# Performance work log

Measured on AMD Instinct MI355X. Metric: run time of the kernel, lower is better.

Reference implementation:

```python
import jax, jax.numpy as jnp
import numpy as np

D_MODEL = 1024
NUM_HEADS = 16
HEAD_WIDTH = 64
SEQ_LEN = 2048
BATCH = 2
NEG_INF = -1e9


def alibi_slopes(num_heads):
    # 2**(-i * 8/num_heads) for i = 1..num_heads, shape [H, 1, 1]
    step = 8.0 / num_heads
    i = jnp.arange(1, num_heads + 1, dtype=jnp.float32)
    return (2.0 ** (-i * step))[:, None, None]


def relative_positions(t_q, t_v):
    # matrix[i, j] = j - i, shape [t_q, t_v]
    return (jnp.arange(t_v)[None, :] - jnp.arange(t_q)[:, None]).astype(jnp.float32)


def setup_inputs() -> dict:
    key = jax.random.key(0)
    ks = jax.random.split(key, 6)
    queries = jax.random.normal(ks[0], (BATCH, SEQ_LEN, D_MODEL), dtype=jnp.float32)
    keys = jax.random.normal(ks[1], (BATCH, SEQ_LEN, D_MODEL), dtype=jnp.float32)
    values = jax.random.normal(ks[2], (BATCH, SEQ_LEN, D_MODEL), dtype=jnp.float32)
    # causal additive mask, broadcastable [1, 1, S, S]
    causal = jnp.where(
        jnp.arange(SEQ_LEN)[None, :] > jnp.arange(SEQ_LEN)[:, None], NEG_INF, 0.0
    ).astype(jnp.float32)[None, None]
    scale = 1.0 / np.sqrt(D_MODEL)
    Wq = jax.random.normal(ks[3], (D_MODEL, D_MODEL), dtype=jnp.float32) * scale
    Wk = jax.random.normal(ks[4], (D_MODEL, D_MODEL), dtype=jnp.float32) * scale
    Wv = jax.random.normal(ks[5], (D_MODEL, D_MODEL), dtype=jnp.float32) * scale
    return {"queries": queries, "keys": keys, "values": values, "mask": causal,
            "Wq": Wq, "Wk": Wk, "Wv": Wv}


def reference(queries, keys, values, mask, Wq, Wk, Wv):
    N, t_q, d = queries.shape
    _, t_v, _ = keys.shape
    H, hw = NUM_HEADS, HEAD_WIDTH

    def split_heads(x, t):
        # [N, t, d] -> [N, H, t, hw]  (nn.Linear: x @ W.T)
        return x.reshape(N, t, H, hw).transpose(0, 2, 1, 3)

    q = split_heads(queries @ Wq.T, t_q)
    k = split_heads(keys @ Wk.T, t_v)
    v = split_heads(values @ Wv.T, t_v)

    att = jnp.einsum("bhqd,bhkd->bhqk", q, k) / np.sqrt(hw)
    # ALiBi bias: slope_h * (j - i), broadcast over batch
    att = att + (alibi_slopes(H) * relative_positions(t_q, t_v))[None]
    att = att + mask[:, :, :t_q, :t_v]
    att = jax.nn.softmax(att, axis=-1)
    res = jnp.einsum("bhqk,bhkd->bhqd", att, v)  # [N, H, t_q, hw]
    return res.transpose(0, 2, 1, 3).reshape(N, t_v, d)
```

## Files before the change

### kernel.cpp

```cpp
#include <hip/hip_runtime.h>
#include <hip/hip_bf16.h>

#define BATCH 2
#define HEADS 16
#define SEQ 2048
#define HW 64
#define DMODEL 1024

typedef unsigned short u16;
typedef __attribute__((ext_vector_type(8))) short short8;
typedef __attribute__((ext_vector_type(4))) float floatx4;

typedef __attribute__((address_space(3))) void* lds_t;
typedef const __attribute__((address_space(1))) void* gbl_t;

__device__ __forceinline__ u16 f2bf(float f) {
    union { float f; unsigned int u; } v; v.f = f;
    unsigned int r = v.u + 0x7fffu + ((v.u >> 16) & 1u);
    return (u16)(r >> 16);
}

__device__ __forceinline__ unsigned int pk2bf(float a, float b) {
    union { __hip_bfloat162 h; unsigned int u; } c;
    c.h = __float22bfloat162_rn(make_float2(a, b));
    return c.u;
}

__global__ __launch_bounds__(256) void proj_kernel(
    const float* __restrict__ Xk, const float* __restrict__ Xv,
    const float* __restrict__ Wk, const float* __restrict__ Wv,
    u16* __restrict__ Ok, u16* __restrict__ Ov)
{
    const float* X; const float* W;
    if (blockIdx.z == 0) { X = Xk; W = Wk; }
    else                 { X = Xv; W = Wv; }

    __shared__ u16 As[128][72];
    __shared__ u16 Bs[128][72];

    const int tid = threadIdx.x;
    const int lane = tid & 63, wave = tid >> 6;
    const int quad = lane >> 4, l15 = lane & 15;
    const int wm = (wave >> 1) << 6, wn = (wave & 1) << 6;
    const int tm = blockIdx.y, tn = blockIdx.x;

    const int sr = tid >> 4;
    const int sc = (tid & 15) << 2;
    const float* Xp = X + (size_t)(tm * 128 + sr) * DMODEL + sc;
    const float* Wp = W + (size_t)(tn * 128 + sr) * DMODEL + sc;

    float4 ra[8], rb[8];
#define PLOAD(K0) \
    for (int i = 0; i < 8; i++) { \
        ra[i] = *reinterpret_cast<const float4*>(Xp + (size_t)16 * i * DMODEL + (K0)); \
        rb[i] = *reinterpret_cast<const float4*>(Wp + (size_t)16 * i * DMODEL + (K0)); \
    }

    floatx4 acc[4][4];
    for (int i = 0; i < 4; i++) for (int j = 0; j < 4; j++) acc[i][j] = (floatx4)0.0f;

    PLOAD(0);
    for (int k0 = 0; k0 < DMODEL; k0 += 64) {
        for (int i = 0; i < 8; i++) {
            uint2 pa; pa.x = pk2bf(ra[i].x, ra[i].y); pa.y = pk2bf(ra[i].z, ra[i].w);
            *reinterpret_cast<uint2*>(&As[sr + 16 * i][sc]) = pa;
            uint2 pb; pb.x = pk2bf(rb[i].x, rb[i].y); pb.y = pk2bf(rb[i].z, rb[i].w);
            *reinterpret_cast<uint2*>(&Bs[sr + 16 * i][sc]) = pb;
        }
        __syncthreads();
        if (k0 + 64 < DMODEL) { PLOAD(k0 + 64); }
        for (int kc = 0; kc < 2; kc++) {
            short8 af[4], bf[4];
            for (int i = 0; i < 4; i++)
                af[i] = *reinterpret_cast<const short8*>(&As[wm + i * 16 + l15][kc * 32 + quad * 8]);
            for (int j = 0; j < 4; j++)
                bf[j] = *reinterpret_cast<const short8*>(&Bs[wn + j * 16 + l15][kc * 32 + quad * 8]);
            for (int i = 0; i < 4; i++)
                for (int j = 0; j < 4; j++)
                    acc[i][j] = __builtin_amdgcn_mfma_f32_16x16x32_bf16(af[i], bf[j], acc[i][j], 0, 0, 0);
        }
        __syncthreads();
    }
#undef PLOAD

    if (blockIdx.z == 0) {
        for (int i = 0; i < 4; i++) for (int j = 0; j < 4; j++) {
            int n = (tn << 7) + wn + (j << 4) + l15;
            int h = n >> 6, d = n & 63;
            for (int r = 0; r < 4; r++) {
                int m = (tm << 7) + wm + (i << 4) + (quad << 2) + r;
                int b = m >> 11, s = m & 2047;
                int pc = (((d >> 3) ^ (s & 7)) << 3) | (d & 7);
                Ok[(size_t)((((b << 4) + h) << 11) + s) * 64 + pc] = f2bf(acc[i][j][r]);
            }
        }
    } else {
        for (int i = 0; i < 4; i++) for (int j = 0; j < 4; j++) {
            int n = (tn << 7) + wn + (j << 4) + l15;
            int h = n >> 6, d = n & 63;
            int m = (tm << 7) + wm + (i << 4) + (quad << 2);
            int b = m >> 11, s0 = m & 2047;
            int ps = (s0 & ~63) | (((((s0 >> 3) & 7) ^ (d & 7)) << 3)) | (s0 & 7);
            uint2 pk;
            pk.x = pk2bf(acc[i][j][0], acc[i][j][1]);
            pk.y = pk2bf(acc[i][j][2], acc[i][j][3]);
            *reinterpret_cast<uint2*>(Ov + ((size_t)(((b << 4) + h) << 6) + d) * SEQ + ps) = pk;
        }
    }
}

__global__ __launch_bounds__(256) void attn_kernel(
    const float* __restrict__ Xq, const float* __restrict__ Wq,
    const u16* __restrict__ K, const u16* __restrict__ VtG,
    float* __restrict__ out)
{
    __shared__ u16 smem[16896];
    u16* Pst = smem + 12288;

    const int tid = threadIdx.x;
    const int lane = tid & 63, wave = tid >> 6;
    const int quad = lane >> 4, l15 = lane & 15;

    const int bid = blockIdx.x;
    const int qt = 31 - (bid >> 5);
    const int bh = bid & 31;
    const int b = bh >> 4, h = bh & 15;
    const float slope = exp2f(-0.5f * (float)(h + 1));
    const int q0 = qt << 6;

    const u16* Kh  = K   + (size_t)bh * SEQ * HW;
    const u16* Vth = VtG + (size_t)bh * HW * SEQ;

#define ISSUE_K(KV, BUF) do { \
    const u16* gk_ = Kh + (size_t)((KV) + wave * 16) * 64 + lane * 8; \
    __builtin_amdgcn_global_load_lds((gbl_t)gk_, (lds_t)(smem + (BUF) * 4096 + wave * 1024), 16, 0, 0); \
    __builtin_amdgcn_global_load_lds((gbl_t)(gk_ + 512), (lds_t)(smem + (BUF) * 4096 + wave * 1024 + 512), 16, 0, 0); \
} while (0)
#define ISSUE_V(KV) do { \
    const u16* gv_ = Vth + (size_t)(wave * 16 + (lane >> 3)) * SEQ + (KV) + (lane & 7) * 8; \
    __builtin_amdgcn_global_load_lds((gbl_t)gv_, (lds_t)(smem + 8192 + wave * 1024), 16, 0, 0); \
    __builtin_amdgcn_global_load_lds((gbl_t)(gv_ + 8 * SEQ), (lds_t)(smem + 8192 + wave * 1024 + 512), 16, 0, 0); \
} while (0)

    {
        u16 (*As)[72] = reinterpret_cast<u16(*)[72]>(smem);
        u16 (*Bs)[72] = reinterpret_cast<u16(*)[72]>(smem + 4608);
        const float* Xb = Xq + (size_t)b * SEQ * DMODEL;
        const float* Wh = Wq + (size_t)h * 64 * DMODEL;
        const int qsr = tid >> 4, qsc = (tid & 15) << 2;
        const float* Xp = Xb + (size_t)(q0 + qsr) * DMODEL + qsc;
        const float* Wp = Wh + (size_t)qsr * DMODEL + qsc;
        float4 qa[4], qw[4];
#define QLOAD(K0) \
        for (int i = 0; i < 4; i++) { \
            qa[i] = *reinterpret_cast<const float4*>(Xp + (size_t)16 * i * DMODEL + (K0)); \
            qw[i] = *reinterpret_cast<const float4*>(Wp + (size_t)16 * i * DMODEL + (K0)); \
        }
        floatx4 accq[4];
        for (int t = 0; t < 4; t++) accq[t] = (floatx4)0.0f;

        QLOAD(0);
        for (int k0 = 0; k0 < DMODEL; k0 += 64) {
            for (int i = 0; i < 4; i++) {
                uint2 pa; pa.x = pk2bf(qa[i].x, qa[i].y); pa.y = pk2bf(qa[i].z, qa[i].w);
                *reinterpret_cast<uint2*>(&As[qsr + 16 * i][qsc]) = pa;
                uint2 pw; pw.x = pk2bf(qw[i].x, qw[i].y); pw.y = pk2bf(qw[i].z, qw[i].w);
                *reinterpret_cast<uint2*>(&Bs[qsr + 16 * i][qsc]) = pw;
            }
            __syncthreads();
            if (k0 + 64 < DMODEL) { QLOAD(k0 + 64); }
            for (int kc = 0; kc < 2; kc++) {
                short8 xa = *reinterpret_cast<const short8*>(&As[wave * 16 + l15][kc * 32 + quad * 8]);
                for (int tn = 0; tn < 4; tn++) {
                    short8 wb = *reinterpret_cast<const short8*>(&Bs[tn * 16 + l15][kc * 32 + quad * 8]);
                    accq[tn] = __builtin_amdgcn_mfma_f32_16x16x32_bf16(xa, wb, accq[tn], 0, 0, 0);
                }
            }
            __syncthreads();
        }
#undef QLOAD
        for (int tn = 0; tn < 4; tn++)
            for (int r = 0; r < 4; r++)
                Pst[wave * 1152 + ((quad << 2) + r) * 72 + tn * 16 + l15] = f2bf(accq[tn][r] * 0.125f);
    }
    short8 qf[2];
    qf[0] = *reinterpret_cast<const short8*>(Pst + wave * 1152 + l15 * 72 + quad * 8);
    qf[1] = *reinterpret_cast<const short8*>(Pst + wave * 1152 + l15 * 72 + 32 + quad * 8);

    ISSUE_K(0, 0);

    const float L2E = 1.44269504088896340736f;
    const float MB  = 12.0f * L2E;
    const int qg = q0 + (wave << 4) + l15;
    const float SL = slope * L2E;
    const int swz = l15 & 7;

    float lpart = 0.0f;
    floatx4 acc_o[4];
    for (int t = 0; t < 4; t++) acc_o[t] = (floatx4)0.0f;

    for (int kt = 0; kt <= qt; kt++) {
        const int kv0 = kt << 6;
        asm volatile("s_waitcnt vmcnt(0)" ::: "memory");
        __syncthreads();
        if (kt < qt) { ISSUE_K(kv0 + 64, (kt + 1) & 1); }
        ISSUE_V(kv0);

        const u16* Kbase = smem + (kt & 1) * 4096;
        floatx4 sv[4];
        for (int t = 0; t < 4; t++) {
            short8 kf0 = *reinterpret_cast<const short8*>(Kbase + (t * 16 + l15) * 64 + ((quad ^ swz) << 3));
            short8 kf1 = *reinterpret_cast<const short8*>(Kbase + (t * 16 + l15) * 64 + (((quad + 4) ^ swz) << 3));
            floatx4 s = (floatx4)0.0f;
            s = __builtin_amdgcn_mfma_f32_16x16x32_bf16(kf0, qf[0], s, 0, 0, 0);
            s = __builtin_amdgcn_mfma_f32_16x16x32_bf16(kf1, qf[1], s, 0, 0, 0);
            sv[t] = s;
        }

        u16* Pt = Pst + wave * 1152;
        if (kt < qt) {
            const float b0 = fmaf(SL, (float)(kv0 + (quad << 2) - qg), -MB);
            for (int t = 0; t < 4; t++) {
                float p0 = __builtin_amdgcn_exp2f(fmaf(sv[t][0], L2E, fmaf(SL, (float)(t * 16 + 0), b0)));
                float p1 = __builtin_amdgcn_exp2f(fmaf(sv[t][1], L2E, fmaf(SL, (float)(t * 16 + 1), b0)));
                float p2 = __builtin_amdgcn_exp2f(fmaf(sv[t][2], L2E, fmaf(SL, (float)(t * 16 + 2), b0)));
                float p3 = __builtin_amdgcn_exp2f(fmaf(sv[t][3], L2E, fmaf(SL, (float)(t * 16 + 3), b0)));
                lpart += (p0 + p1) + (p2 + p3);
                uint2 pk; pk.x = pk2bf(p0, p1); pk.y = pk2bf(p2, p3);
                *reinterpret_cast<uint2*>(Pt + l15 * 72 + t * 16 + (quad << 2)) = pk;
            }
        } else {
            const float fb = (float)(kv0 + (quad << 2) - qg);
            for (int t = 0; t < 4; t++) {
                float p[4];
                for (int r = 0; r < 4; r++) {
                    float rel = fb + (float)(t * 16 + r);
                    float bd = fmaf(fminf(slope * rel, -1e9f * rel), L2E, -MB);
                    p[r] = __builtin_amdgcn_exp2f(fmaf(sv[t][r], L2E, bd));
                }
                lpart += (p[0] + p[1]) + (p[2] + p[3]);
                uint2 pk; pk.x = pk2bf(p[0], p[1]); pk.y = pk2bf(p[2], p[3]);
                *reinterpret_cast<uint2*>(Pt + l15 * 72 + t * 16 + (quad << 2)) = pk;
            }
        }

        asm volatile("s_waitcnt vmcnt(0)" ::: "memory");
        __syncthreads();

        short8 pf0 = *reinterpret_cast<const short8*>(Pt + l15 * 72 + quad * 8);
        short8 pf1 = *reinterpret_cast<const short8*>(Pt + l15 * 72 + 32 + quad * 8);
        for (int t2 = 0; t2 < 4; t2++) {
            short8 vf0 = *reinterpret_cast<const short8*>(smem + 8192 + (t2 * 16 + l15) * 64 + ((quad ^ swz) << 3));
            short8 vf1 = *reinterpret_cast<const short8*>(smem + 8192 + (t2 * 16 + l15) * 64 + (((quad + 4) ^ swz) << 3));
            acc_o[t2] = __builtin_amdgcn_mfma_f32_16x16x32_bf16(vf0, pf0, acc_o[t2], 0, 0, 0);
            acc_o[t2] = __builtin_amdgcn_mfma_f32_16x16x32_bf16(vf1, pf1, acc_o[t2], 0, 0, 0);
        }
    }
#undef ISSUE_K
#undef ISSUE_V

    float l_run = lpart;
    l_run += __shfl_xor(l_run, 16);
    l_run += __shfl_xor(l_run, 32);
    const float inv = 1.0f / l_run;

    float* op = out + (size_t)(b * SEQ + qg) * DMODEL + h * 64;
    for (int t2 = 0; t2 < 4; t2++) {
        float4 o;
        o.x = acc_o[t2][0] * inv; o.y = acc_o[t2][1] * inv;
        o.z = acc_o[t2][2] * inv; o.w = acc_o[t2][3] * inv;
        *reinterpret_cast<float4*>(op + t2 * 16 + (quad << 2)) = o;
    }
}

extern "C" void kernel_launch(void* const* d_in, const int* in_sizes, int n_in,
                              void* d_out, int out_size, void* d_ws, size_t ws_size,
                              hipStream_t stream) {
    const float* q  = (const float*)d_in[0];
    const float* k  = (const float*)d_in[1];
    const float* v  = (const float*)d_in[2];
    const float* wq = (const float*)d_in[4];
    const float* wk = (const float*)d_in[5];
    const float* wv = (const float*)d_in[6];
    float* out = (float*)d_out;

    const size_t headElems = (size_t)BATCH * HEADS * SEQ * HW;
    u16* Kb  = (u16*)d_ws;
    u16* VtB = Kb + headElems;

    dim3 pgrid(DMODEL / 128, (BATCH * SEQ) / 128, 2);
    proj_kernel<<<pgrid, 256, 0, stream>>>(k, v, wk, wv, Kb, VtB);
    attn_kernel<<<BATCH * HEADS * (SEQ / 64), 256, 0, stream>>>(q, wq, Kb, VtB, out);
}
```

Baseline: 199.9 us.

## Move Q projection into proj kernel and relax attention loop barriers

Q projection is now computed by the shared projection GEMM (as a third grid slice) into a swizzled bf16 workspace, with the attention scale folded in. The attention kernel then loads Q tiles straight into LDS instead of redoing a small GEMM per block. The attention loop also replaces __syncthreads with raw s_barrier plus partial vmcnt waits, issues V before the next K prefetch, and raises wave priority around the MFMA sections. This costs extra workspace and a bf16 write and read of Q, and the partial waits rely on exact load ordering.

```diff
diff --git a/kernel.cpp b/kernel.cpp
--- a/kernel.cpp
+++ b/kernel.cpp
@@ -27,13 +27,14 @@
 }
 
 __global__ __launch_bounds__(256) void proj_kernel(
-    const float* __restrict__ Xk, const float* __restrict__ Xv,
-    const float* __restrict__ Wk, const float* __restrict__ Wv,
-    u16* __restrict__ Ok, u16* __restrict__ Ov)
+    const float* __restrict__ Xk, const float* __restrict__ Xv, const float* __restrict__ Xq,
+    const float* __restrict__ Wk, const float* __restrict__ Wv, const float* __restrict__ Wq,
+    u16* __restrict__ Ok, u16* __restrict__ Ov, u16* __restrict__ Oq)
 {
     const float* X; const float* W;
-    if (blockIdx.z == 0) { X = Xk; W = Wk; }
-    else                 { X = Xv; W = Wv; }
+    if (blockIdx.z == 0)      { X = Xk; W = Wk; }
+    else if (blockIdx.z == 1) { X = Xv; W = Wv; }
+    else                      { X = Xq; W = Wq; }
 
     __shared__ u16 As[128][72];
     __shared__ u16 Bs[128][72];
@@ -83,7 +84,9 @@
     }
 #undef PLOAD
 
-    if (blockIdx.z == 0) {
+    if (blockIdx.z != 1) {
+        u16* O = (blockIdx.z == 0) ? Ok : Oq;
+        const float mul = (blockIdx.z == 0) ? 1.0f : 0.125f;
         for (int i = 0; i < 4; i++) for (int j = 0; j < 4; j++) {
             int n = (tn << 7) + wn + (j << 4) + l15;
             int h = n >> 6, d = n & 63;
@@ -91,7 +94,7 @@
                 int m = (tm << 7) + wm + (i << 4) + (quad << 2) + r;
                 int b = m >> 11, s = m & 2047;
                 int pc = (((d >> 3) ^ (s & 7)) << 3) | (d & 7);
-                Ok[(size_t)((((b << 4) + h) << 11) + s) * 64 + pc] = f2bf(acc[i][j][r]);
+                O[(size_t)((((b << 4) + h) << 11) + s) * 64 + pc] = f2bf(acc[i][j][r] * mul);
             }
         }
     } else {
@@ -110,9 +113,8 @@
 }
 
 __global__ __launch_bounds__(256) void attn_kernel(
-    const float* __restrict__ Xq, const float* __restrict__ Wq,
-    const u16* __restrict__ K, const u16* __restrict__ VtG,
-    float* __restrict__ out)
+    const u16* __restrict__ Qg, const u16* __restrict__ K,
+    const u16* __restrict__ VtG, float* __restrict__ out)
 {
     __shared__ u16 smem[16896];
     u16* Pst = smem + 12288;
@@ -127,7 +129,9 @@
     const int b = bh >> 4, h = bh & 15;
     const float slope = exp2f(-0.5f * (float)(h + 1));
     const int q0 = qt << 6;
-
+    const int swz = l15 & 7;
+
+    const u16* Qh  = Qg  + (size_t)bh * SEQ * HW;
     const u16* Kh  = K   + (size_t)bh * SEQ * HW;
     const u16* Vth = VtG + (size_t)bh * HW * SEQ;
 
@@ -143,49 +147,16 @@
 } while (0)
 
     {
-        u16 (*As)[72] = reinterpret_cast<u16(*)[72]>(smem);
-        u16 (*Bs)[72] = reinterpret_cast<u16(*)[72]>(smem + 4608);
-        const float* Xb = Xq + (size_t)b * SEQ * DMODEL;
-        const float* Wh = Wq + (size_t)h * 64 * DMODEL;
-        const int qsr = tid >> 4, qsc = (tid & 15) << 2;
-        const float* Xp = Xb + (size_t)(q0 + qsr) * DMODEL + qsc;
-        const float* Wp = Wh + (size_t)qsr * DMODEL + qsc;
-        float4 qa[4], qw[4];
-#define QLOAD(K0) \
-        for (int i = 0; i < 4; i++) { \
-            qa[i] = *reinterpret_cast<const float4*>(Xp + (size_t)16 * i * DMODEL + (K0)); \
-            qw[i] = *reinterpret_cast<const float4*>(Wp + (size_t)16 * i * DMODEL + (K0)); \
-        }
-        floatx4 accq[4];
-        for (int t = 0; t < 4; t++) accq[t] = (floatx4)0.0f;
-
-        QLOAD(0);
-        for (int k0 = 0; k0 < DMODEL; k0 += 64) {
-            for (int i = 0; i < 4; i++) {
-                uint2 pa; pa.x = pk2bf(qa[i].x, qa[i].y); pa.y = pk2bf(qa[i].z, qa[i].w);
-                *reinterpret_cast<uint2*>(&As[qsr + 16 * i][qsc]) = pa;
-                uint2 pw; pw.x = pk2bf(qw[i].x, qw[i].y); pw.y = pk2bf(qw[i].z, qw[i].w);
-                *reinterpret_cast<uint2*>(&Bs[qsr + 16 * i][qsc]) = pw;
-            }
-            __syncthreads();
-            if (k0 + 64 < DMODEL) { QLOAD(k0 + 64); }
-            for (int kc = 0; kc < 2; kc++) {
-                short8 xa = *reinterpret_cast<const short8*>(&As[wave * 16 + l15][kc * 32 + quad * 8]);
-                for (int tn = 0; tn < 4; tn++) {
-                    short8 wb = *reinterpret_cast<const short8*>(&Bs[tn * 16 + l15][kc * 32 + quad * 8]);
-                    accq[tn] = __builtin_amdgcn_mfma_f32_16x16x32_bf16(xa, wb, accq[tn], 0, 0, 0);
-                }
-            }
-            __syncthreads();
-        }
-#undef QLOAD
-        for (int tn = 0; tn < 4; tn++)
-            for (int r = 0; r < 4; r++)
-                Pst[wave * 1152 + ((quad << 2) + r) * 72 + tn * 16 + l15] = f2bf(accq[tn][r] * 0.125f);
-    }
+        const u16* gq = Qh + (size_t)(q0 + wave * 16) * 64 + lane * 8;
+        __builtin_amdgcn_global_load_lds((gbl_t)gq, (lds_t)(smem + 8192 + wave * 1024), 16, 0, 0);
+        __builtin_amdgcn_global_load_lds((gbl_t)(gq + 512), (lds_t)(smem + 8192 + wave * 1024 + 512), 16, 0, 0);
+    }
+    asm volatile("s_waitcnt vmcnt(0)" ::: "memory");
     short8 qf[2];
-    qf[0] = *reinterpret_cast<const short8*>(Pst + wave * 1152 + l15 * 72 + quad * 8);
-    qf[1] = *reinterpret_cast<const short8*>(Pst + wave * 1152 + l15 * 72 + 32 + quad * 8);
+    qf[0] = *reinterpret_cast<const short8*>(smem + 8192 + (wave * 16 + l15) * 64 + ((quad ^ swz) << 3));
+    qf[1] = *reinterpret_cast<const short8*>(smem + 8192 + (wave * 16 + l15) * 64 + (((quad + 4) ^ swz) << 3));
+    asm volatile("s_waitcnt lgkmcnt(0)" ::: "memory");
+    __builtin_amdgcn_sched_barrier(0);
 
     ISSUE_K(0, 0);
 
@@ -193,7 +164,6 @@
     const float MB  = 12.0f * L2E;
     const int qg = q0 + (wave << 4) + l15;
     const float SL = slope * L2E;
-    const int swz = l15 & 7;
 
     float lpart = 0.0f;
     floatx4 acc_o[4];
@@ -202,12 +172,14 @@
     for (int kt = 0; kt <= qt; kt++) {
         const int kv0 = kt << 6;
         asm volatile("s_waitcnt vmcnt(0)" ::: "memory");
-        __syncthreads();
+        __builtin_amdgcn_s_barrier();
+        __builtin_amdgcn_sched_barrier(0);
+        ISSUE_V(kv0);
         if (kt < qt) { ISSUE_K(kv0 + 64, (kt + 1) & 1); }
-        ISSUE_V(kv0);
 
         const u16* Kbase = smem + (kt & 1) * 4096;
         floatx4 sv[4];
+        __builtin_amdgcn_s_setprio(1);
         for (int t = 0; t < 4; t++) {
             short8 kf0 = *reinterpret_cast<const short8*>(Kbase + (t * 16 + l15) * 64 + ((quad ^ swz) << 3));
             short8 kf1 = *reinterpret_cast<const short8*>(Kbase + (t * 16 + l15) * 64 + (((quad + 4) ^ swz) << 3));
@@ -216,6 +188,7 @@
             s = __builtin_amdgcn_mfma_f32_16x16x32_bf16(kf1, qf[1], s, 0, 0, 0);
             sv[t] = s;
         }
+        __builtin_amdgcn_s_setprio(0);
 
         u16* Pt = Pst + wave * 1152;
         if (kt < qt) {
@@ -244,17 +217,21 @@
             }
         }
 
-        asm volatile("s_waitcnt vmcnt(0)" ::: "memory");
-        __syncthreads();
+        if (kt < qt) { asm volatile("s_waitcnt vmcnt(2)" ::: "memory"); }
+        else         { asm volatile("s_waitcnt vmcnt(0)" ::: "memory"); }
+        __builtin_amdgcn_s_barrier();
+        __builtin_amdgcn_sched_barrier(0);
 
         short8 pf0 = *reinterpret_cast<const short8*>(Pt + l15 * 72 + quad * 8);
         short8 pf1 = *reinterpret_cast<const short8*>(Pt + l15 * 72 + 32 + quad * 8);
+        __builtin_amdgcn_s_setprio(1);
         for (int t2 = 0; t2 < 4; t2++) {
             short8 vf0 = *reinterpret_cast<const short8*>(smem + 8192 + (t2 * 16 + l15) * 64 + ((quad ^ swz) << 3));
             short8 vf1 = *reinterpret_cast<const short8*>(smem + 8192 + (t2 * 16 + l15) * 64 + (((quad + 4) ^ swz) << 3));
             acc_o[t2] = __builtin_amdgcn_mfma_f32_16x16x32_bf16(vf0, pf0, acc_o[t2], 0, 0, 0);
             acc_o[t2] = __builtin_amdgcn_mfma_f32_16x16x32_bf16(vf1, pf1, acc_o[t2], 0, 0, 0);
         }
+        __builtin_amdgcn_s_setprio(0);
     }
 #undef ISSUE_K
 #undef ISSUE_V
@@ -287,8 +264,9 @@
     const size_t headElems = (size_t)BATCH * HEADS * SEQ * HW;
     u16* Kb  = (u16*)d_ws;
     u16* VtB = Kb + headElems;
-
-    dim3 pgrid(DMODEL / 128, (BATCH * SEQ) / 128, 2);
-    proj_kernel<<<pgrid, 256, 0, stream>>>(k, v, wk, wv, Kb, VtB);
-    attn_kernel<<<BATCH * HEADS * (SEQ / 64), 256, 0, stream>>>(q, wq, Kb, VtB, out);
-}
+    u16* Qb  = VtB + headElems;
+
+    dim3 pgrid(DMODEL / 128, (BATCH * SEQ) / 128, 3);
+    proj_kernel<<<pgrid, 256, 0, stream>>>(k, v, q, wk, wv, wq, Kb, VtB, Qb);
+    attn_kernel<<<BATCH * HEADS * (SEQ / 64), 256, 0, stream>>>(Qb, Kb, VtB, out);
+}
```

Measured after the change: 206.6 us. 1.03x slower.
